# Kernel optimization log

Measured on AMD Instinct MI355X. Metric: run time of the kernel, lower is better.

Reference implementation:

```python
import jax, jax.numpy as jnp
import numpy as np

B, N, DIM = 64, 197, 768
H = 12
IN_DIM = 768
HD = IN_DIM // H  # 64


def setup_inputs() -> dict:
    key = jax.random.key(0)
    k1, k2, k3 = jax.random.split(key, 3)
    x = jax.random.normal(k1, (B, N, DIM), dtype=jnp.float32)
    # learnable per-head scale, initialized to head_dim**-0.5
    scale = (DIM // H) ** (-0.5) * jnp.ones((H,), dtype=jnp.float32)
    w_qkv = jax.random.normal(k2, (3 * IN_DIM, DIM), dtype=jnp.float32) * 0.02  # qkv_bias=False
    w_proj = jax.random.normal(k3, (IN_DIM, IN_DIM), dtype=jnp.float32) * 0.02
    b_proj = jnp.zeros((IN_DIM,), dtype=jnp.float32)
    return {"x": x, "scale": scale, "w_qkv": w_qkv, "w_proj": w_proj, "b_proj": b_proj}


def reference(x, scale, w_qkv, w_proj, b_proj):
    Bx, Nx, C = x.shape
    # qkv projection -> [3, B, H, N, HD]
    qkv = jnp.einsum('bnc,oc->bno', x, w_qkv).reshape(Bx, Nx, 3, H, HD)
    qkv = qkv.transpose(2, 0, 3, 1, 4)
    q, k, v = qkv[0], qkv[1], qkv[2]
    # per-head learnable scale (LMSA)
    attn = jnp.einsum('bhid,bhjd->bhij', q, k) * scale[None, :, None, None]
    # diagonal mask -> -inf (self-token masking)
    diag = jnp.eye(Nx, dtype=bool)  # [N, N]
    attn = jnp.where(diag[None, None, :, :], -jnp.inf, attn)
    attn = jax.nn.softmax(attn, axis=-1)
    out = jnp.einsum('bhij,bhjd->bhid', attn, v)  # [B, H, N, HD]
    out = out.transpose(0, 2, 1, 3).reshape(Bx, Nx, IN_DIM)
    out = out @ w_proj.T + b_proj
    return out + x  # num_heads > 1 branch: residual add
```

## Files before the change

kernel.cpp:

```cpp
#include <hip/hip_runtime.h>
#include <cstdint>
#include <cstddef>

#define DEV static __device__ __forceinline__

typedef __attribute__((ext_vector_type(8))) short bf16x8;
typedef __attribute__((ext_vector_type(4))) float f32x4;

constexpr int NB   = 64;
constexpr int NTOK = 197;
constexpr int DIMC = 768;
constexpr int NH   = 12;
constexpr int HDIM = 64;
constexpr int MTOK = NB * NTOK;
constexpr int QKVO = 3 * DIMC;
constexpr int BH   = NB * NH;
constexpr int KROWS = 198;
constexpr int VTS   = 232;
constexpr int OBS   = 68;
constexpr int GM64  = MTOK / 64;

constexpr int GMQ  = (MTOK + 127) / 128;
constexpr int GNQ  = QKVO / 128;
constexpr int NKT  = DIMC / 64;
constexpr int HBUF = 16384;

constexpr int PBUF = 12288;

DEV unsigned short f2bf(float f) {
  union { float f; uint32_t u; } v; v.f = f;
  uint32_t u = v.u;
  return (unsigned short)((u + 0x7FFFu + ((u >> 16) & 1u)) >> 16);
}

DEV uint32_t pack_bf2(float a, float b) {
  uint32_t r;
  asm("v_cvt_pk_bf16_f32 %0, %1, %2" : "=v"(r) : "v"(a), "v"(b));
  return r;
}

DEV f32x4 mfma16(bf16x8 a, bf16x8 b, f32x4 c) {
  return __builtin_amdgcn_mfma_f32_16x16x32_bf16(a, b, c, 0, 0, 0);
}

DEV void async_cp16(const unsigned short* g, unsigned short* l) {
  __builtin_amdgcn_global_load_lds(
      (__attribute__((address_space(1))) void*)g,
      (__attribute__((address_space(3))) void*)l, 16, 0, 0);
}

DEV void swizzle_idx(int lin, int gridM, int gridN, int& mt, int& nt) {
  int per = 16 * gridN;
  int sup = lin / per;
  int bm  = sup * 16;
  int Gm  = gridM - bm; if (Gm > 16) Gm = 16;
  int rem = lin - sup * per;
  nt = rem / Gm;
  mt = bm + (rem - nt * Gm);
}

constexpr int CVB1 = (MTOK * DIMC) / 4096;
constexpr int CVB2 = (QKVO * DIMC) / 4096;
constexpr int CVB3 = (DIMC * DIMC) / 4096;
constexpr int CVNB = CVB1 + CVB2 + CVB3;

__global__ void __launch_bounds__(256) cvt_all(const float* __restrict__ x,
                                               const float* __restrict__ wq,
                                               const float* __restrict__ wp,
                                               unsigned short* __restrict__ xb,
                                               unsigned short* __restrict__ wqb,
                                               unsigned short* __restrict__ wpb) {
  int blk = blockIdx.x;
  const float* s; unsigned short* d;
  if (blk < CVB1)               { s = x;  d = xb; }
  else if (blk < CVB1 + CVB2)   { s = wq; d = wqb; blk -= CVB1; }
  else                          { s = wp; d = wpb; blk -= CVB1 + CVB2; }
  size_t base = (size_t)blk * 4096 + (size_t)threadIdx.x * 4;
#pragma unroll
  for (int j = 0; j < 4; ++j) {
    size_t i = base + (size_t)j * 1024;
    float4 f = *(const float4*)(s + i);
    ushort4 o;
    o.x = f2bf(f.x); o.y = f2bf(f.y); o.z = f2bf(f.z); o.w = f2bf(f.w);
    *(ushort4*)(d + i) = o;
  }
}

DEV void stage_mat(const unsigned short* src, unsigned short* dst,
                   int rbase, int k0, int clampR, int tid) {
#pragma unroll
  for (int u = 0; u < 4; ++u) {
    int c = u * 256 + tid;
    int row = c >> 3, cc = c & 7;
    int gr = rbase + row; gr = gr < clampR ? gr : clampR - 1;
    int gc = (cc ^ (row & 7)) * 8;
    async_cp16(src + (size_t)gr * DIMC + k0 + gc, dst + c * 8);
  }
}

template <int KK>
DEV void ldAB(const unsigned short* Ac, const unsigned short* Bc,
              int wm, int wn, int l16, int quad,
              bf16x8 (&af)[4], bf16x8 (&bf_)[4]) {
#pragma unroll
  for (int mi = 0; mi < 4; ++mi) {
    int r = wm * 64 + mi * 16 + l16;
    af[mi] = *(const bf16x8*)(Ac + r * 64 + (((KK * 4 + quad) ^ (r & 7)) * 8));
  }
#pragma unroll
  for (int ni = 0; ni < 4; ++ni) {
    int r = wn * 64 + ni * 16 + l16;
    bf_[ni] = *(const bf16x8*)(Bc + r * 64 + (((KK * 4 + quad) ^ (r & 7)) * 8));
  }
}

DEV void mm16(bf16x8 (&af)[4], bf16x8 (&bf_)[4], f32x4 (&acc)[4][4]) {
  __builtin_amdgcn_s_setprio(1);
#pragma unroll
  for (int mi = 0; mi < 4; ++mi)
#pragma unroll
    for (int ni = 0; ni < 4; ++ni)
      acc[mi][ni] = mfma16(af[mi], bf_[ni], acc[mi][ni]);
  __builtin_amdgcn_s_setprio(0);
}

__global__ void __launch_bounds__(256, 2) gemm_qkv(const unsigned short* __restrict__ A,
                                                   const unsigned short* __restrict__ Bw,
                                                   unsigned short* __restrict__ qkv) {
  extern __shared__ unsigned short lds[];
  const int tid = threadIdx.x, lane = tid & 63, wave = tid >> 6;
  const int wm = wave & 1, wn = wave >> 1;
  const int l16 = lane & 15, quad = lane >> 4;
  int mt, nt;
  swizzle_idx(blockIdx.x, GMQ, GNQ, mt, nt);
  const int mbase = mt * 128, nbase = nt * 128;

  f32x4 acc[4][4];
#pragma unroll
  for (int i = 0; i < 4; ++i)
#pragma unroll
    for (int j = 0; j < 4; ++j) acc[i][j] = {0.f, 0.f, 0.f, 0.f};

  unsigned short* A0 = lds;
  unsigned short* B0 = lds + 8192;
  unsigned short* A1 = lds + HBUF;
  unsigned short* B1 = lds + HBUF + 8192;

  stage_mat(A,  A0, mbase, 0, MTOK, tid);
  stage_mat(Bw, B0, nbase, 0, QKVO, tid);
  asm volatile("s_waitcnt vmcnt(0)" ::: "memory");
  __builtin_amdgcn_s_barrier();

  for (int kt = 0; kt < NKT; ++kt) {
    const unsigned short* Ac = (kt & 1) ? A1 : A0;
    const unsigned short* Bc = (kt & 1) ? B1 : B0;
    unsigned short* An = (kt & 1) ? A0 : A1;
    unsigned short* Bn = (kt & 1) ? B0 : B1;

    if (kt + 1 < NKT) {
      int k0n = (kt + 1) * 64;
      stage_mat(A,  An, mbase, k0n, MTOK, tid);
      stage_mat(Bw, Bn, nbase, k0n, QKVO, tid);
    }

    bf16x8 af[4], bf_[4];
    ldAB<0>(Ac, Bc, wm, wn, l16, quad, af, bf_);
    mm16(af, bf_, acc);
    ldAB<1>(Ac, Bc, wm, wn, l16, quad, af, bf_);
    mm16(af, bf_, acc);

    if (kt + 1 < NKT) {
      asm volatile("s_waitcnt vmcnt(0)" ::: "memory");
      __builtin_amdgcn_s_barrier();
    }
  }

  const int oc64  = nbase + wn * 64;
  const int which = oc64 / DIMC;
  const int h     = (oc64 % DIMC) / HDIM;
#pragma unroll
  for (int mi = 0; mi < 4; ++mi) {
    int t0 = mbase + wm * 64 + mi * 16 + quad * 4;
#pragma unroll
    for (int r = 0; r < 4; ++r) {
      int t = t0 + r;
      if (t < MTOK) {
        int b = t / NTOK, n = t - b * NTOK;
        size_t base = ((size_t)((which * NB + b) * NH + h) * NTOK + n) * HDIM;
#pragma unroll
        for (int ni = 0; ni < 4; ++ni)
          qkv[base + ni * 16 + l16] = f2bf(acc[mi][ni][r]);
      }
    }
  }
}

DEV void stage_proj(const unsigned short* A, const unsigned short* Bw,
                    unsigned short* Abuf, unsigned short* Bbuf,
                    int mbase, int nbase, int k0, int tid) {
#pragma unroll
  for (int i = 0; i < 2; ++i) {
    int c = i * 256 + tid;
    int row = c >> 3, cc = c & 7;
    int gc = (cc ^ (row & 7)) * 8;
    async_cp16(A + (size_t)(mbase + row) * DIMC + k0 + gc, Abuf + c * 8);
  }
#pragma unroll
  for (int i = 0; i < 4; ++i) {
    int c = i * 256 + tid;
    int row = c >> 3, cc = c & 7;
    int gc = (cc ^ (row & 7)) * 8;
    async_cp16(Bw + (size_t)(nbase + row) * DIMC + k0 + gc, Bbuf + c * 8);
  }
}

__global__ void __launch_bounds__(256, 3) gemm_proj(const unsigned short* __restrict__ A,
                                                    const unsigned short* __restrict__ Bw,
                                                    const float* __restrict__ bias,
                                                    const float* __restrict__ xres,
                                                    float* __restrict__ out) {
  extern __shared__ unsigned short lds[];
  const int tid = threadIdx.x, lane = tid & 63, wave = tid >> 6;
  const int wm = wave & 1, wn = wave >> 1;
  const int l16 = lane & 15, quad = lane >> 4;
  int mt, nt;
  swizzle_idx(blockIdx.x, GM64, DIMC / 128, mt, nt);
  const int mbase = mt * 64, nbase = nt * 128;

  f32x4 acc[2][4];
#pragma unroll
  for (int i = 0; i < 2; ++i)
#pragma unroll
    for (int j = 0; j < 4; ++j) acc[i][j] = {0.f, 0.f, 0.f, 0.f};

  unsigned short* A0 = lds;
  unsigned short* B0 = lds + 4096;
  unsigned short* A1 = lds + PBUF;
  unsigned short* B1 = lds + PBUF + 4096;

  stage_proj(A, Bw, A0, B0, mbase, nbase, 0, tid);
  asm volatile("s_waitcnt vmcnt(0)" ::: "memory");
  __builtin_amdgcn_s_barrier();

  for (int kt = 0; kt < NKT; ++kt) {
    const unsigned short* Ac = (kt & 1) ? A1 : A0;
    const unsigned short* Bc = (kt & 1) ? B1 : B0;
    unsigned short* An = (kt & 1) ? A0 : A1;
    unsigned short* Bn = (kt & 1) ? B0 : B1;

    if (kt + 1 < NKT)
      stage_proj(A, Bw, An, Bn, mbase, nbase, (kt + 1) * 64, tid);

#pragma unroll
    for (int kk = 0; kk < 64; kk += 32) {
      const int cw = (kk >> 3) + quad;
      bf16x8 af[2], bfr[4];
#pragma unroll
      for (int mi = 0; mi < 2; ++mi) {
        int r = wm * 32 + mi * 16 + l16;
        af[mi] = *(const bf16x8*)(Ac + r * 64 + ((cw ^ (r & 7)) * 8));
      }
#pragma unroll
      for (int ni = 0; ni < 4; ++ni) {
        int r = wn * 64 + ni * 16 + l16;
        bfr[ni] = *(const bf16x8*)(Bc + r * 64 + ((cw ^ (r & 7)) * 8));
      }
      __builtin_amdgcn_s_setprio(1);
#pragma unroll
      for (int mi = 0; mi < 2; ++mi)
#pragma unroll
        for (int ni = 0; ni < 4; ++ni)
          acc[mi][ni] = mfma16(af[mi], bfr[ni], acc[mi][ni]);
      __builtin_amdgcn_s_setprio(0);
    }

    if (kt + 1 < NKT) {
      asm volatile("s_waitcnt vmcnt(0)" ::: "memory");
      __builtin_amdgcn_s_barrier();
    }
  }

  const int oc = nbase + wn * 64;
#pragma unroll
  for (int mi = 0; mi < 2; ++mi) {
    int t0 = mbase + wm * 32 + mi * 16 + quad * 4;
#pragma unroll
    for (int r = 0; r < 4; ++r) {
      int t = t0 + r;
      size_t rowb = (size_t)t * DIMC;
#pragma unroll
      for (int ni = 0; ni < 4; ++ni) {
        int o = oc + ni * 16 + l16;
        out[rowb + o] = acc[mi][ni][r] + bias[o] + xres[rowb + o];
      }
    }
  }
}

__global__ void __launch_bounds__(512, 2) attn_fused(const unsigned short* __restrict__ qkv,
                                                     const float* __restrict__ scale,
                                                     unsigned short* __restrict__ aout) {
  __shared__ __align__(16) unsigned short Ks[KROWS * 64];
  __shared__ __align__(16) unsigned short Vt[HDIM * VTS];
  __shared__ __align__(16) unsigned short Ob[8 * 16 * OBS];

  const int tid = threadIdx.x, lane = tid & 63, wave = tid >> 6;
  const int l16 = lane & 15, quad = lane >> 4;
  const int bh = blockIdx.x;
  const int b = bh / NH, h = bh - b * NH;

  const unsigned short* qg = qkv + (size_t)bh * (NTOK * HDIM);
  const unsigned short* kg = qkv + (size_t)(BH + bh) * (NTOK * HDIM);
  const unsigned short* vg = qkv + (size_t)(2 * BH + bh) * (NTOK * HDIM);
  const float sc = scale[h];

#pragma unroll
  for (int i = 0; i < 4; ++i) {
    int c = i * 512 + tid;
    if (c < KROWS * 8) {
      int row = c >> 3, cc = c & 7;
      async_cp16(kg + (size_t)row * 64 + ((cc ^ (row & 7)) * 8), Ks + c * 8);
    }
  }
  {
    const int dcol = tid & 63;
    const int slab = tid >> 6;
#pragma unroll
    for (int p = 0; p < 4; ++p) {
      int n0 = p * 64 + slab * 8;
      if (n0 + 8 <= VTS) {
        union { unsigned short us[8]; bf16x8 v; } tr;
#pragma unroll
        for (int i = 0; i < 8; ++i) {
          int n = n0 + i; n = n > NTOK - 1 ? NTOK - 1 : n;
          tr.us[i] = vg[(size_t)n * HDIM + dcol];
        }
        *(bf16x8*)(Vt + dcol * VTS + n0) = tr.v;
      }
    }
  }
  __syncthreads();

  const int srcA  = l16 + ((quad & 1) << 5);
  const int srcB  = srcA + 16;
  const int stsel = quad >> 1;
  unsigned short* ob = Ob + wave * (16 * OBS);

  for (int mt = wave; mt < 13; mt += 8) {
    int qr = mt * 16 + l16; if (qr > NTOK - 1) qr = NTOK - 1;
    bf16x8 qb0 = *(const bf16x8*)(qg + (size_t)qr * 64 + quad * 8);
    bf16x8 qb1 = *(const bf16x8*)(qg + (size_t)qr * 64 + 32 + quad * 8);
    const int mg = mt * 16 + l16;

    f32x4 s[7][2];
#pragma unroll
    for (int jc = 0; jc < 7; ++jc)
#pragma unroll
      for (int st = 0; st < 2; ++st) {
        if (jc == 6 && st == 1) { s[6][1] = {0.f, 0.f, 0.f, 0.f}; continue; }
        int jrow = (jc * 2 + st) * 16 + l16;
        jrow = jrow > NTOK ? NTOK : jrow;
        const unsigned short* kr = Ks + jrow * 64;
        bf16x8 ka0 = *(const bf16x8*)(kr + (quad       ^ (jrow & 7)) * 8);
        bf16x8 ka1 = *(const bf16x8*)(kr + ((4 + quad) ^ (jrow & 7)) * 8);
        f32x4 t = {0.f, 0.f, 0.f, 0.f};
        t = mfma16(ka0, qb0, t);
        t = mfma16(ka1, qb1, t);
        s[jc][st] = t;
      }

    float cmax = -1e30f;
#pragma unroll
    for (int jc = 0; jc < 7; ++jc)
#pragma unroll
      for (int st = 0; st < 2; ++st)
#pragma unroll
        for (int r = 0; r < 4; ++r) {
          int jg = jc * 32 + st * 16 + quad * 4 + r;
          float v = s[jc][st][r] * sc;
          v = (jg >= NTOK || jg == mg) ? -1e30f : v;
          s[jc][st][r] = v;
          cmax = fmaxf(cmax, v);
        }
    cmax = fmaxf(cmax, __shfl_xor(cmax, 16));
    cmax = fmaxf(cmax, __shfl_xor(cmax, 32));
    float psum = 0.f;
#pragma unroll
    for (int jc = 0; jc < 7; ++jc)
#pragma unroll
      for (int st = 0; st < 2; ++st)
#pragma unroll
        for (int r = 0; r < 4; ++r) {
          float e = __expf(s[jc][st][r] - cmax);
          psum += e;
          s[jc][st][r] = e;
        }
    psum += __shfl_xor(psum, 16);
    psum += __shfl_xor(psum, 32);
    const float inv = 1.0f / psum;

    f32x4 oacc[4];
#pragma unroll
    for (int dt = 0; dt < 4; ++dt) oacc[dt] = {0.f, 0.f, 0.f, 0.f};

#pragma unroll
    for (int jc = 0; jc < 7; ++jc) {
      uint32_t u0 = pack_bf2(s[jc][0][0], s[jc][0][1]);
      uint32_t v0 = pack_bf2(s[jc][0][2], s[jc][0][3]);
      uint32_t u1 = pack_bf2(s[jc][1][0], s[jc][1][1]);
      uint32_t v1 = pack_bf2(s[jc][1][2], s[jc][1][3]);
      uint32_t au0 = (uint32_t)__shfl((int)u0, srcA);
      uint32_t av0 = (uint32_t)__shfl((int)v0, srcA);
      uint32_t au1 = (uint32_t)__shfl((int)u1, srcA);
      uint32_t av1 = (uint32_t)__shfl((int)v1, srcA);
      uint32_t bu0 = (uint32_t)__shfl((int)u0, srcB);
      uint32_t bv0 = (uint32_t)__shfl((int)v0, srcB);
      uint32_t bu1 = (uint32_t)__shfl((int)u1, srcB);
      uint32_t bv1 = (uint32_t)__shfl((int)v1, srcB);
      union { uint32_t u[4]; bf16x8 v; } pb;
      pb.u[0] = stsel ? au1 : au0;
      pb.u[1] = stsel ? av1 : av0;
      pb.u[2] = stsel ? bu1 : bu0;
      pb.u[3] = stsel ? bv1 : bv0;
#pragma unroll
      for (int dt = 0; dt < 4; ++dt) {
        bf16x8 va = *(const bf16x8*)(Vt + (dt * 16 + l16) * VTS +
                                     jc * 32 + quad * 8);
        oacc[dt] = mfma16(va, pb.v, oacc[dt]);
      }
    }

#pragma unroll
    for (int dt = 0; dt < 4; ++dt) {
      uint2 pk;
      pk.x = pack_bf2(oacc[dt][0] * inv, oacc[dt][1] * inv);
      pk.y = pack_bf2(oacc[dt][2] * inv, oacc[dt][3] * inv);
      *(uint2*)(ob + l16 * OBS + dt * 16 + quad * 4) = pk;
    }
    __asm__ __volatile__("s_waitcnt lgkmcnt(0)" ::: "memory");
#pragma unroll
    for (int rnd = 0; rnd < 4; ++rnd) {
      int q   = rnd * 4 + (lane >> 4);
      int o8  = lane & 15;
      uint2 d8 = *(const uint2*)(ob + q * OBS + o8 * 4);
      int qrow = mt * 16 + q;
      if (qrow < NTOK) {
        size_t obase = (size_t)(b * NTOK + qrow) * DIMC + h * HDIM;
        *(uint2*)(aout + obase + o8 * 4) = d8;
      }
    }
  }
}

extern "C" void kernel_launch(void* const* d_in, const int* in_sizes, int n_in,
                              void* d_out, int out_size, void* d_ws, size_t ws_size,
                              hipStream_t stream) {
  const float* x     = (const float*)d_in[0];
  const float* scale = (const float*)d_in[1];
  const float* wqkv  = (const float*)d_in[2];
  const float* wproj = (const float*)d_in[3];
  const float* bproj = (const float*)d_in[4];
  float* out = (float*)d_out;

  unsigned short* xb   = (unsigned short*)d_ws;
  unsigned short* wqb  = xb  + (size_t)MTOK * DIMC;
  unsigned short* wpb  = wqb + (size_t)QKVO * DIMC;
  unsigned short* qkvb = wpb + (size_t)DIMC * DIMC;
  unsigned short* attb = xb;

  static bool attr_set = false;
  if (!attr_set) {
    hipFuncSetAttribute(reinterpret_cast<const void*>(gemm_qkv),
                        hipFuncAttributeMaxDynamicSharedMemorySize, 65536);
    hipFuncSetAttribute(reinterpret_cast<const void*>(gemm_proj),
                        hipFuncAttributeMaxDynamicSharedMemorySize, 49152);
    attr_set = true;
  }

  cvt_all<<<CVNB, 256, 0, stream>>>(x, wqkv, wproj, xb, wqb, wpb);
  gemm_qkv<<<GMQ * GNQ, 256, 65536, stream>>>(xb, wqb, qkvb);
  attn_fused<<<BH, 512, 0, stream>>>(qkvb, scale, attb);
  gemm_proj<<<GM64 * (DIMC / 128), 256, 49152, stream>>>(attb, wpb, bproj, x, out);
}
```

Measured before the change: 198.2 us.

## Triple-buffer QKV GEMM with K=32 stages and raise occupancy to three blocks

The QKV projection GEMM moves from double-buffered K=64 tiles to triple-buffered K=32 tiles, keeping two async loads in flight with a partial vmcnt wait instead of draining all loads each step. LDS per block drops from 64KB to 48KB and launch bounds go to 3 blocks per CU, so more waves can hide latency. The cost is twice as many barriers and K iterations, a denser two-rows-per-LDS-row swizzle, and possible register pressure from the higher occupancy target.

```diff
diff --git a/kernel.cpp b/kernel.cpp
--- a/kernel.cpp
+++ b/kernel.cpp
@@ -23,7 +23,8 @@
 constexpr int GMQ  = (MTOK + 127) / 128;
 constexpr int GNQ  = QKVO / 128;
 constexpr int NKT  = DIMC / 64;
-constexpr int HBUF = 16384;
+constexpr int NKT2 = DIMC / 32;
+constexpr int QBUF = 8192;
 
 constexpr int PBUF = 12288;
 
@@ -86,31 +87,36 @@
   }
 }
 
-DEV void stage_mat(const unsigned short* src, unsigned short* dst,
-                   int rbase, int k0, int clampR, int tid) {
-#pragma unroll
-  for (int u = 0; u < 4; ++u) {
-    int c = u * 256 + tid;
-    int row = c >> 3, cc = c & 7;
-    int gr = rbase + row; gr = gr < clampR ? gr : clampR - 1;
-    int gc = (cc ^ (row & 7)) * 8;
-    async_cp16(src + (size_t)gr * DIMC + k0 + gc, dst + c * 8);
-  }
-}
-
-template <int KK>
-DEV void ldAB(const unsigned short* Ac, const unsigned short* Bc,
-              int wm, int wn, int l16, int quad,
-              bf16x8 (&af)[4], bf16x8 (&bf_)[4]) {
+DEV void stage_mat32(const unsigned short* src, unsigned short* dst,
+                     int rbase, int k0, int clampR, int tid) {
+#pragma unroll
+  for (int u2 = 0; u2 < 2; ++u2) {
+    int c = u2 * 256 + tid;
+    int row2 = c >> 3, slot = c & 7;
+    int ccl = slot ^ (row2 & 7);
+    int r = (row2 << 1) | (ccl >> 2);
+    int u = ccl & 3;
+    int gr = rbase + r; gr = gr < clampR ? gr : clampR - 1;
+    async_cp16(src + (size_t)gr * DIMC + k0 + u * 8, dst + c * 8);
+  }
+}
+
+DEV void ldAB32(const unsigned short* Ac, const unsigned short* Bc,
+                int wm, int wn, int l16, int quad,
+                bf16x8 (&af)[4], bf16x8 (&bf_)[4]) {
 #pragma unroll
   for (int mi = 0; mi < 4; ++mi) {
     int r = wm * 64 + mi * 16 + l16;
-    af[mi] = *(const bf16x8*)(Ac + r * 64 + (((KK * 4 + quad) ^ (r & 7)) * 8));
+    int row2 = r >> 1;
+    int slot = (((r & 1) << 2) | quad) ^ (row2 & 7);
+    af[mi] = *(const bf16x8*)(Ac + row2 * 64 + slot * 8);
   }
 #pragma unroll
   for (int ni = 0; ni < 4; ++ni) {
     int r = wn * 64 + ni * 16 + l16;
-    bf_[ni] = *(const bf16x8*)(Bc + r * 64 + (((KK * 4 + quad) ^ (r & 7)) * 8));
+    int row2 = r >> 1;
+    int slot = (((r & 1) << 2) | quad) ^ (row2 & 7);
+    bf_[ni] = *(const bf16x8*)(Bc + row2 * 64 + slot * 8);
   }
 }
 
@@ -124,7 +130,7 @@
   __builtin_amdgcn_s_setprio(0);
 }
 
-__global__ void __launch_bounds__(256, 2) gemm_qkv(const unsigned short* __restrict__ A,
+__global__ void __launch_bounds__(256, 3) gemm_qkv(const unsigned short* __restrict__ A,
                                                    const unsigned short* __restrict__ Bw,
                                                    unsigned short* __restrict__ qkv) {
   extern __shared__ unsigned short lds[];
@@ -141,38 +147,34 @@
 #pragma unroll
     for (int j = 0; j < 4; ++j) acc[i][j] = {0.f, 0.f, 0.f, 0.f};
 
-  unsigned short* A0 = lds;
-  unsigned short* B0 = lds + 8192;
-  unsigned short* A1 = lds + HBUF;
-  unsigned short* B1 = lds + HBUF + 8192;
-
-  stage_mat(A,  A0, mbase, 0, MTOK, tid);
-  stage_mat(Bw, B0, nbase, 0, QKVO, tid);
-  asm volatile("s_waitcnt vmcnt(0)" ::: "memory");
+  unsigned short *Ar  = lds,              *Br  = lds + 4096;
+  unsigned short *An1 = lds + QBUF,       *Bn1 = lds + QBUF + 4096;
+  unsigned short *An2 = lds + 2 * QBUF,   *Bn2 = lds + 2 * QBUF + 4096;
+
+  stage_mat32(A,  Ar,  mbase, 0,  MTOK, tid);
+  stage_mat32(Bw, Br,  nbase, 0,  QKVO, tid);
+  stage_mat32(A,  An1, mbase, 32, MTOK, tid);
+  stage_mat32(Bw, Bn1, nbase, 32, QKVO, tid);
+  asm volatile("s_waitcnt vmcnt(8)" ::: "memory");
   __builtin_amdgcn_s_barrier();
 
-  for (int kt = 0; kt < NKT; ++kt) {
-    const unsigned short* Ac = (kt & 1) ? A1 : A0;
-    const unsigned short* Bc = (kt & 1) ? B1 : B0;
-    unsigned short* An = (kt & 1) ? A0 : A1;
-    unsigned short* Bn = (kt & 1) ? B0 : B1;
-
-    if (kt + 1 < NKT) {
-      int k0n = (kt + 1) * 64;
-      stage_mat(A,  An, mbase, k0n, MTOK, tid);
-      stage_mat(Bw, Bn, nbase, k0n, QKVO, tid);
+  for (int kt = 0; kt < NKT2; ++kt) {
+    if (kt + 2 < NKT2) {
+      int k0n = (kt + 2) * 32;
+      stage_mat32(A,  An2, mbase, k0n, MTOK, tid);
+      stage_mat32(Bw, Bn2, nbase, k0n, QKVO, tid);
     }
 
     bf16x8 af[4], bf_[4];
-    ldAB<0>(Ac, Bc, wm, wn, l16, quad, af, bf_);
+    ldAB32(Ar, Br, wm, wn, l16, quad, af, bf_);
     mm16(af, bf_, acc);
-    ldAB<1>(Ac, Bc, wm, wn, l16, quad, af, bf_);
-    mm16(af, bf_, acc);
-
-    if (kt + 1 < NKT) {
-      asm volatile("s_waitcnt vmcnt(0)" ::: "memory");
-      __builtin_amdgcn_s_barrier();
-    }
+
+    if (kt + 2 < NKT2)      asm volatile("s_waitcnt vmcnt(8)" ::: "memory");
+    else if (kt + 1 < NKT2) asm volatile("s_waitcnt vmcnt(0)" ::: "memory");
+    if (kt + 1 < NKT2) __builtin_amdgcn_s_barrier();
+
+    unsigned short* ta = Ar; Ar = An1; An1 = An2; An2 = ta;
+    unsigned short* tb = Br; Br = Bn1; Bn1 = Bn2; Bn2 = tb;
   }
 
   const int oc64  = nbase + wn * 64;
@@ -471,14 +473,14 @@
   static bool attr_set = false;
   if (!attr_set) {
     hipFuncSetAttribute(reinterpret_cast<const void*>(gemm_qkv),
-                        hipFuncAttributeMaxDynamicSharedMemorySize, 65536);
+                        hipFuncAttributeMaxDynamicSharedMemorySize, 49152);
     hipFuncSetAttribute(reinterpret_cast<const void*>(gemm_proj),
                         hipFuncAttributeMaxDynamicSharedMemorySize, 49152);
     attr_set = true;
   }
 
   cvt_all<<<CVNB, 256, 0, stream>>>(x, wqkv, wproj, xb, wqb, wpb);
-  gemm_qkv<<<GMQ * GNQ, 256, 65536, stream>>>(xb, wqb, qkvb);
+  gemm_qkv<<<GMQ * GNQ, 256, 49152, stream>>>(xb, wqb, qkvb);
   attn_fused<<<BH, 512, 0, stream>>>(qkvb, scale, attb);
   gemm_proj<<<GM64 * (DIMC / 128), 256, 49152, stream>>>(attb, wpb, bproj, x, out);
 }
```

After: 205.9 us. +3.9%, slower.

## Fuse x fp32-to-bf16 conversion into QKV GEMM A-tile staging

Applied to the files above, without the earlier changes.

The QKV GEMM now reads fp32 x directly through registers, converts it to bf16 and writes it into LDS, instead of relying on a separate conversion pass that wrote a bf16 copy of x. This removes a full read and write of the activation tensor and shrinks the conversion kernel to the weights only. In exchange, each GEMM block reads twice the bytes for A (fp32), A no longer uses async global-to-LDS copies, and x tiles are re-converted by every N-tile block. Register pressure rises from holding the prefetched fp32 values, and the vmcnt(4) wait ordering depends on how the compiler orders the loads.

```diff
diff --git a/kernel.cpp b/kernel.cpp
--- a/kernel.cpp
+++ b/kernel.cpp
@@ -59,22 +59,18 @@
   mt = bm + (rem - nt * Gm);
 }
 
-constexpr int CVB1 = (MTOK * DIMC) / 4096;
 constexpr int CVB2 = (QKVO * DIMC) / 4096;
 constexpr int CVB3 = (DIMC * DIMC) / 4096;
-constexpr int CVNB = CVB1 + CVB2 + CVB3;
-
-__global__ void __launch_bounds__(256) cvt_all(const float* __restrict__ x,
-                                               const float* __restrict__ wq,
+constexpr int CVNB = CVB2 + CVB3;
+
+__global__ void __launch_bounds__(256) cvt_all(const float* __restrict__ wq,
                                                const float* __restrict__ wp,
-                                               unsigned short* __restrict__ xb,
                                                unsigned short* __restrict__ wqb,
                                                unsigned short* __restrict__ wpb) {
   int blk = blockIdx.x;
   const float* s; unsigned short* d;
-  if (blk < CVB1)               { s = x;  d = xb; }
-  else if (blk < CVB1 + CVB2)   { s = wq; d = wqb; blk -= CVB1; }
-  else                          { s = wp; d = wpb; blk -= CVB1 + CVB2; }
+  if (blk < CVB2) { s = wq; d = wqb; }
+  else            { s = wp; d = wpb; blk -= CVB2; }
   size_t base = (size_t)blk * 4096 + (size_t)threadIdx.x * 4;
 #pragma unroll
   for (int j = 0; j < 4; ++j) {
@@ -86,15 +82,41 @@
   }
 }
 
-DEV void stage_mat(const unsigned short* src, unsigned short* dst,
-                   int rbase, int k0, int clampR, int tid) {
+DEV void stage_A_load(const float* __restrict__ X, int mbase, int k0, int tid,
+                      float4 (&ld)[4][2]) {
 #pragma unroll
   for (int u = 0; u < 4; ++u) {
     int c = u * 256 + tid;
     int row = c >> 3, cc = c & 7;
-    int gr = rbase + row; gr = gr < clampR ? gr : clampR - 1;
+    int gr = mbase + row; gr = gr < MTOK ? gr : MTOK - 1;
     int gc = (cc ^ (row & 7)) * 8;
-    async_cp16(src + (size_t)gr * DIMC + k0 + gc, dst + c * 8);
+    const float* p = X + (size_t)gr * DIMC + k0 + gc;
+    ld[u][0] = *(const float4*)(p);
+    ld[u][1] = *(const float4*)(p + 4);
+  }
+}
+
+DEV void stage_A_write(unsigned short* dst, int tid, float4 (&ld)[4][2]) {
+#pragma unroll
+  for (int u = 0; u < 4; ++u) {
+    int c = u * 256 + tid;
+    uint4 w;
+    w.x = pack_bf2(ld[u][0].x, ld[u][0].y);
+    w.y = pack_bf2(ld[u][0].z, ld[u][0].w);
+    w.z = pack_bf2(ld[u][1].x, ld[u][1].y);
+    w.w = pack_bf2(ld[u][1].z, ld[u][1].w);
+    *(uint4*)(dst + c * 8) = w;
+  }
+}
+
+DEV void stage_B(const unsigned short* src, unsigned short* dst,
+                 int rbase, int k0, int tid) {
+#pragma unroll
+  for (int u = 0; u < 4; ++u) {
+    int c = u * 256 + tid;
+    int row = c >> 3, cc = c & 7;
+    int gc = (cc ^ (row & 7)) * 8;
+    async_cp16(src + (size_t)(rbase + row) * DIMC + k0 + gc, dst + c * 8);
   }
 }
 
@@ -124,7 +146,7 @@
   __builtin_amdgcn_s_setprio(0);
 }
 
-__global__ void __launch_bounds__(256, 2) gemm_qkv(const unsigned short* __restrict__ A,
+__global__ void __launch_bounds__(256, 2) gemm_qkv(const float* __restrict__ X,
                                                    const unsigned short* __restrict__ Bw,
                                                    unsigned short* __restrict__ qkv) {
   extern __shared__ unsigned short lds[];
@@ -146,9 +168,13 @@
   unsigned short* A1 = lds + HBUF;
   unsigned short* B1 = lds + HBUF + 8192;
 
-  stage_mat(A,  A0, mbase, 0, MTOK, tid);
-  stage_mat(Bw, B0, nbase, 0, QKVO, tid);
-  asm volatile("s_waitcnt vmcnt(0)" ::: "memory");
+  float4 ald[4][2];
+
+  stage_A_load(X, mbase, 0, tid, ald);
+  stage_B(Bw, B0, nbase, 0, tid);
+  asm volatile("s_waitcnt vmcnt(4)" ::: "memory");
+  stage_A_write(A0, tid, ald);
+  asm volatile("s_waitcnt vmcnt(0) lgkmcnt(0)" ::: "memory");
   __builtin_amdgcn_s_barrier();
 
   for (int kt = 0; kt < NKT; ++kt) {
@@ -159,8 +185,8 @@
 
     if (kt + 1 < NKT) {
       int k0n = (kt + 1) * 64;
-      stage_mat(A,  An, mbase, k0n, MTOK, tid);
-      stage_mat(Bw, Bn, nbase, k0n, QKVO, tid);
+      stage_A_load(X, mbase, k0n, tid, ald);
+      stage_B(Bw, Bn, nbase, k0n, tid);
     }
 
     bf16x8 af[4], bf_[4];
@@ -170,7 +196,9 @@
     mm16(af, bf_, acc);
 
     if (kt + 1 < NKT) {
-      asm volatile("s_waitcnt vmcnt(0)" ::: "memory");
+      asm volatile("s_waitcnt vmcnt(4)" ::: "memory");
+      stage_A_write(An, tid, ald);
+      asm volatile("s_waitcnt vmcnt(0) lgkmcnt(0)" ::: "memory");
       __builtin_amdgcn_s_barrier();
     }
   }
@@ -477,8 +505,8 @@
     attr_set = true;
   }
 
-  cvt_all<<<CVNB, 256, 0, stream>>>(x, wqkv, wproj, xb, wqb, wpb);
-  gemm_qkv<<<GMQ * GNQ, 256, 65536, stream>>>(xb, wqb, qkvb);
+  cvt_all<<<CVNB, 256, 0, stream>>>(wqkv, wproj, wqb, wpb);
+  gemm_qkv<<<GMQ * GNQ, 256, 65536, stream>>>(x, wqb, qkvb);
   attn_fused<<<BH, 512, 0, stream>>>(qkvb, scale, attb);
   gemm_proj<<<GM64 * (DIMC / 128), 256, 49152, stream>>>(attb, wpb, bproj, x, out);
 }
```

New measurement: 213.9 us. 1.08x slower.
